# Kernel tuning notes

Hardware: AMD Instinct MI355X
Metric: run time of the kernel (lower is better)

## Reference

```python
import jax, jax.numpy as jnp
import numpy as np

B, N, D, K = 16, 512, 256, 12  # batch, nodes, node_dim, num edge types (4 arg + 4 arg' + punct +/- + no_edges +/-)
ITERATION_STEPS = 1


def setup_inputs() -> dict:
    key = jax.random.key(0)
    ks = jax.random.split(key, 8)
    node = jax.random.normal(ks[0], (B, N, D), dtype=jnp.float32)
    node_mask = jax.random.randint(ks[1], (B, N), 0, 2, dtype=jnp.int32)
    graphs = jax.random.randint(ks[2], (K, B, N, N), 0, 2, dtype=jnp.int32)
    s = 1.0 / np.sqrt(D)
    Ww = jax.random.normal(ks[3], (1, D), dtype=jnp.float32) * s   # _node_weight_fc
    bw = jnp.zeros((1,), dtype=jnp.float32)
    Ws = jax.random.normal(ks[4], (D, D), dtype=jnp.float32) * s   # _self_node_fc
    bs = jnp.zeros((D,), dtype=jnp.float32)
    Wk = jax.random.normal(ks[5], (K, D, D), dtype=jnp.float32) * s  # 12 bias-free per-edge-type linears
    return {"node": node, "Ww": Ww, "bw": bw, "Ws": Ws, "bs": bs, "Wk": Wk,
            "node_mask": node_mask, "graphs": graphs}


def reference(node, Ww, bw, Ws, bs, Wk, node_mask, graphs):
    dt = node.dtype
    mask = node_mask.astype(dt)
    eye = jnp.eye(N, dtype=dt)
    # dd_graph = mask_row * mask_col * (1 - diag)
    dd = mask[:, None, :] * mask[:, :, None] * (1.0 - eye)          # [B,N,N]
    g = dd[None] * graphs.astype(dt)                                # [K,B,N,N] masked adjacencies
    neigh = g.sum(axis=(0, 3))                                      # [B,N] total neighbor count
    neigh = jnp.where(neigh >= 1, neigh, jnp.ones((), dt))

    all_w = []
    for _ in range(ITERATION_STEPS):
        # (1) node relatedness
        w = jax.nn.sigmoid(node @ Ww.T + bw)[..., 0]                # [B,N]
        all_w.append(w)
        self_info = node @ Ws.T + bs                                # [B,N,D]
        # (2) message propagation for all 12 edge types, batched
        trans = jnp.einsum('bnd,ked->kbne', node, Wk)               # [K,B,N,D] per-type linear (x @ W.T)
        wg = w[None, :, None, :] * g                                # [K,B,N,N] masked node weights
        agg = jnp.einsum('kbmn,kbnd->bmd', wg, trans) / neigh[..., None]
        # (3) update
        node = jax.nn.relu(self_info + agg)

    all_weight = jnp.stack(all_w, axis=1)                           # [B,steps,N]
    return node, all_weight
```

## Files before the change

### kernel.cpp

```cpp
#include <hip/hip_runtime.h>
#include <hip/hip_bf16.h>
#include <math.h>

#define BB 16
#define NN 512
#define DD 256
#define KK 12

typedef __bf16 bf16x8 __attribute__((ext_vector_type(8)));
typedef __bf16 bf16x4 __attribute__((ext_vector_type(4)));
typedef float  f32x4  __attribute__((ext_vector_type(4)));

#define WS_WM     0
#define WS_NCNT   32768
#define WS_NODEBF 65536
#define WS_NODET  4259840
#define WS_WKBF   8454144
#define WS_WSBF   10027008
#define WS_T      10158080

__global__ __launch_bounds__(256) void k1_prep(const float* __restrict__ node,
        const float* __restrict__ Ww, const float* __restrict__ bw,
        const int* __restrict__ node_mask,
        float* __restrict__ wm, __bf16* __restrict__ node_bf,
        float* __restrict__ all_w) {
    int t = threadIdx.x;
    int lane = t & 63;
    int row = blockIdx.x * 4 + (t >> 6);
    const float4 nv = *(const float4*)(node + (size_t)row * DD + lane * 4);
    const float4 wv = *(const float4*)(Ww + lane * 4);
    float dot = nv.x*wv.x + nv.y*wv.y + nv.z*wv.z + nv.w*wv.w;
    #pragma unroll
    for (int off = 32; off > 0; off >>= 1) dot += __shfl_xor(dot, off);
    float w = 1.0f / (1.0f + expf(-(dot + bw[0])));
    int mk = node_mask[row];
    if (lane == 0) {
        wm[row]    = w * (float)mk;
        all_w[row] = w;
    }
    bf16x4 nb = {(__bf16)nv.x, (__bf16)nv.y, (__bf16)nv.z, (__bf16)nv.w};
    *(bf16x4*)(node_bf + (size_t)row * DD + lane * 4) = nb;
}

__global__ __launch_bounds__(256) void k1b_convert(const float* __restrict__ Wk,
        const float* __restrict__ Ws, __bf16* __restrict__ Wk_bf, __bf16* __restrict__ Ws_bf) {
    const int KDD = KK * DD * DD;
    int idx = (blockIdx.x * 256 + threadIdx.x) * 4;
    if (idx < KDD) {
        float4 v = *(const float4*)(Wk + idx);
        bf16x4 o = {(__bf16)v.x, (__bf16)v.y, (__bf16)v.z, (__bf16)v.w};
        *(bf16x4*)(Wk_bf + idx) = o;
    } else {
        int j = idx - KDD;
        if (j < DD * DD) {
            float4 v = *(const float4*)(Ws + j);
            bf16x4 o = {(__bf16)v.x, (__bf16)v.y, (__bf16)v.z, (__bf16)v.w};
            *(bf16x4*)(Ws_bf + j) = o;
        }
    }
}

__global__ __launch_bounds__(256) void k2_transpose(const float* __restrict__ node,
        const float* __restrict__ wm, __bf16* __restrict__ dst) {
    __shared__ float tile[64][65];
    int bx = blockIdx.x;
    int b = bx >> 5; int rest = bx & 31; int nt = rest >> 2; int dt = rest & 3;
    int n0 = nt * 64, d0 = dt * 64;
    int t = threadIdx.x;
    #pragma unroll
    for (int i = 0; i < 16; i++) {
        int idx = i * 256 + t;
        int n = idx >> 6, d = idx & 63;
        tile[n][d] = node[((size_t)(b * NN + n0 + n)) * DD + d0 + d];
    }
    __syncthreads();
    #pragma unroll
    for (int i = 0; i < 16; i++) {
        int idx = i * 256 + t;
        int d = idx >> 6, n = idx & 63;
        float w = wm[b * NN + n0 + n];
        dst[((size_t)(b * DD + d0 + d)) * NN + n0 + n] = (__bf16)(tile[n][d] * w);
    }
}

__global__ __launch_bounds__(256) void k4_stageA(const int* __restrict__ graphs,
        const int* __restrict__ node_mask, const __bf16* __restrict__ node_t,
        __bf16* __restrict__ T, int* __restrict__ ncnt) {
    __shared__ __align__(16) __bf16 Asub[64][72];
    int bx = blockIdx.x;
    int mt = bx & 7;
    int kb = bx >> 3;
    int b = kb & 15;
    int k = kb >> 4;
    int m0 = mt * 64;
    int t = threadIdx.x;
    int lane = t & 63;
    int wave = t >> 6;
    int q = lane >> 4;
    int l16 = lane & 15;
    int e0 = wave * 64;

    f32x4 acc[4][4];
    #pragma unroll
    for (int i = 0; i < 4; i++)
        #pragma unroll
        for (int j = 0; j < 4; j++) acc[i][j] = (f32x4){0.f, 0.f, 0.f, 0.f};

    int am = t >> 2;
    int aq = t & 3;
    const int* grow = graphs + ((size_t)((k * BB + b) * NN + m0 + am)) * NN;
    const int* mrow = node_mask + b * NN;
    int mg = m0 + am;
    unsigned cnt = 0;

    for (int n0 = 0; n0 < NN; n0 += 64) {
        #pragma unroll
        for (int i = 0; i < 4; i++) {
            int nbase = n0 + aq * 16 + i * 4;
            int4 g  = *(const int4*)(grow + nbase);
            int4 mk = *(const int4*)(mrow + nbase);
            unsigned p0 = (unsigned)g.x | ((unsigned)g.y << 16);
            unsigned p1 = (unsigned)g.z | ((unsigned)g.w << 16);
            unsigned drel = (unsigned)(mg - nbase);
            if (drel < 4u) {
                unsigned bit = 1u << (16 * (drel & 1));
                if (drel < 2u) p0 &= ~bit; else p1 &= ~bit;
            }
            unsigned mp0 = (unsigned)mk.x | ((unsigned)mk.y << 16);
            unsigned mp1 = (unsigned)mk.z | ((unsigned)mk.w << 16);
            cnt += (p0 & mp0) + (p1 & mp1);
            uint2 st;
            st.x = p0 * 0x3F80u;
            st.y = p1 * 0x3F80u;
            *(uint2*)&Asub[am][aq * 16 + i * 4] = st;
        }
        __syncthreads();
        #pragma unroll
        for (int kk = 0; kk < 2; kk++) {
            bf16x8 af[4], bfr[4];
            #pragma unroll
            for (int fm = 0; fm < 4; fm++)
                af[fm] = *(const bf16x8*)&Asub[fm * 16 + l16][kk * 32 + q * 8];
            #pragma unroll
            for (int fd = 0; fd < 4; fd++)
                bfr[fd] = *(const bf16x8*)(node_t +
                    ((size_t)(b * DD + e0 + fd * 16 + l16)) * NN + n0 + kk * 32 + q * 8);
            #pragma unroll
            for (int fm = 0; fm < 4; fm++)
                #pragma unroll
                for (int fd = 0; fd < 4; fd++)
                    acc[fm][fd] = __builtin_amdgcn_mfma_f32_16x16x32_bf16(
                        af[fm], bfr[fd], acc[fm][fd], 0, 0, 0);
        }
        __syncthreads();
    }

    cnt = (cnt & 0xFFFFu) + (cnt >> 16);
    int ci = (int)cnt;
    ci += __shfl_xor(ci, 1);
    ci += __shfl_xor(ci, 2);
    if (aq == 0) atomicAdd(&ncnt[b * NN + mg], ci);

    #pragma unroll
    for (int fm = 0; fm < 4; fm++)
        #pragma unroll
        for (int fd = 0; fd < 4; fd++) {
            int col = e0 + fd * 16 + l16;
            #pragma unroll
            for (int r = 0; r < 4; r++) {
                int m = m0 + fm * 16 + q * 4 + r;
                T[((size_t)((b * NN + m) * KK + k)) * DD + col] = (__bf16)acc[fm][fd][r];
            }
        }
}

__global__ __launch_bounds__(256) void k5_stageB(const __bf16* __restrict__ T,
        const __bf16* __restrict__ Wk_bf, const __bf16* __restrict__ node_bf,
        const __bf16* __restrict__ Ws_bf, const float* __restrict__ bs,
        const int* __restrict__ ncnt, const int* __restrict__ node_mask,
        float* __restrict__ out) {
    __shared__ float redbuf[64][65];
    int bx = blockIdx.x;
    int b = bx >> 5; int rest = bx & 31; int mt = rest >> 2; int dt = rest & 3;
    int m0 = mt * 64, d0 = dt * 64;
    int t = threadIdx.x;
    int lane = t & 63;
    int wave = t >> 6;
    int q = lane >> 4;
    int l16 = lane & 15;
    int ew = wave * 64;

    f32x4 acc[4][4];
    #pragma unroll
    for (int i = 0; i < 4; i++)
        #pragma unroll
        for (int j = 0; j < 4; j++) acc[i][j] = (f32x4){0.f, 0.f, 0.f, 0.f};

    for (int k = 0; k < KK; k++) {
        #pragma unroll
        for (int kk = 0; kk < 2; kk++) {
            int eoff = ew + kk * 32 + q * 8;
            bf16x8 af[4], bfr[4];
            #pragma unroll
            for (int fm = 0; fm < 4; fm++)
                af[fm] = *(const bf16x8*)(T +
                    ((size_t)(b * NN + m0 + fm * 16 + l16)) * (KK * DD) + k * DD + eoff);
            #pragma unroll
            for (int fd = 0; fd < 4; fd++)
                bfr[fd] = *(const bf16x8*)(Wk_bf +
                    ((size_t)(k * DD + d0 + fd * 16 + l16)) * DD + eoff);
            #pragma unroll
            for (int fm = 0; fm < 4; fm++)
                #pragma unroll
                for (int fd = 0; fd < 4; fd++)
                    acc[fm][fd] = __builtin_amdgcn_mfma_f32_16x16x32_bf16(
                        af[fm], bfr[fd], acc[fm][fd], 0, 0, 0);
        }
    }

    #pragma unroll
    for (int fm = 0; fm < 4; fm++) {
        #pragma unroll
        for (int r = 0; r < 4; r++) {
            int m = m0 + fm * 16 + q * 4 + r;
            int c = ncnt[b * NN + m];
            float s = (float)node_mask[b * NN + m] / (float)(c >= 1 ? c : 1);
            #pragma unroll
            for (int fd = 0; fd < 4; fd++) acc[fm][fd][r] *= s;
        }
    }

    #pragma unroll
    for (int kk = 0; kk < 2; kk++) {
        int eoff = ew + kk * 32 + q * 8;
        bf16x8 af[4], bfr[4];
        #pragma unroll
        for (int fm = 0; fm < 4; fm++)
            af[fm] = *(const bf16x8*)(node_bf +
                ((size_t)(b * NN + m0 + fm * 16 + l16)) * DD + eoff);
        #pragma unroll
        for (int fd = 0; fd < 4; fd++)
            bfr[fd] = *(const bf16x8*)(Ws_bf +
                ((size_t)(d0 + fd * 16 + l16)) * DD + eoff);
        #pragma unroll
        for (int fm = 0; fm < 4; fm++)
            #pragma unroll
            for (int fd = 0; fd < 4; fd++)
                acc[fm][fd] = __builtin_amdgcn_mfma_f32_16x16x32_bf16(
                    af[fm], bfr[fd], acc[fm][fd], 0, 0, 0);
    }

    for (int w = 0; w < 4; w++) {
        if (wave == w) {
            #pragma unroll
            for (int fm = 0; fm < 4; fm++)
                #pragma unroll
                for (int fd = 0; fd < 4; fd++) {
                    int dd2 = fd * 16 + l16;
                    #pragma unroll
                    for (int r = 0; r < 4; r++) {
                        int mm = fm * 16 + q * 4 + r;
                        if (w == 0) redbuf[mm][dd2] = acc[fm][fd][r];
                        else        redbuf[mm][dd2] += acc[fm][fd][r];
                    }
                }
        }
        __syncthreads();
    }

    int row = t >> 2;
    int c0 = (t & 3) * 16;
    #pragma unroll
    for (int j = 0; j < 4; j++) {
        int d = d0 + c0 + j * 4;
        float4 bv = *(const float4*)(bs + d);
        float4 v;
        v.x = fmaxf(redbuf[row][c0 + j * 4 + 0] + bv.x, 0.0f);
        v.y = fmaxf(redbuf[row][c0 + j * 4 + 1] + bv.y, 0.0f);
        v.z = fmaxf(redbuf[row][c0 + j * 4 + 2] + bv.z, 0.0f);
        v.w = fmaxf(redbuf[row][c0 + j * 4 + 3] + bv.w, 0.0f);
        *(float4*)(out + ((size_t)(b * NN + m0 + row)) * DD + d) = v;
    }
}

extern "C" void kernel_launch(void* const* d_in, const int* in_sizes, int n_in,
                              void* d_out, int out_size, void* d_ws, size_t ws_size,
                              hipStream_t stream) {
    const float* node      = (const float*)d_in[0];
    const float* Ww        = (const float*)d_in[1];
    const float* bw        = (const float*)d_in[2];
    const float* Ws        = (const float*)d_in[3];
    const float* bs        = (const float*)d_in[4];
    const float* Wk        = (const float*)d_in[5];
    const int*   node_mask = (const int*)d_in[6];
    const int*   graphs    = (const int*)d_in[7];
    float* out   = (float*)d_out;
    float* all_w = out + (size_t)BB * NN * DD;

    char* ws = (char*)d_ws;
    float*  wm      = (float*)(ws + WS_WM);
    int*    ncnt    = (int*)(ws + WS_NCNT);
    __bf16* node_bf = (__bf16*)(ws + WS_NODEBF);
    __bf16* node_t  = (__bf16*)(ws + WS_NODET);
    __bf16* Wk_bf   = (__bf16*)(ws + WS_WKBF);
    __bf16* Ws_bf   = (__bf16*)(ws + WS_WSBF);
    __bf16* Tbuf    = (__bf16*)(ws + WS_T);

    hipMemsetAsync(ncnt, 0, BB * NN * sizeof(int), stream);
    k1_prep    <<<2048, 256, 0, stream>>>(node, Ww, bw, node_mask, wm, node_bf, all_w);
    k1b_convert<<< 832, 256, 0, stream>>>(Wk, Ws, Wk_bf, Ws_bf);
    k2_transpose<<<512, 256, 0, stream>>>(node, wm, node_t);
    k4_stageA  <<<1536, 256, 0, stream>>>(graphs, node_mask, node_t, Tbuf, ncnt);
    k5_stageB  <<< 512, 256, 0, stream>>>(Tbuf, Wk_bf, node_bf, Ws_bf, bs, ncnt, node_mask, out);
}
```

Baseline: 393.2 us.

## Stage full adjacency row block in LDS upfront and count neighbors via MFMA

Stage A now loads the whole 64x512 masked adjacency tile for a block into shared memory in one pass, using wide coalesced int4 loads with eight loads in flight. After a single barrier it runs all 16 MFMA k-steps without per-chunk syncs. The per-row neighbor count, previously a scalar popcount-style sum against node_mask, is now an extra MFMA against a bf16 mask vector spread across waves and reduced through LDS. Block index order is also changed so the batch index varies fastest. In exchange the kernel uses about 66KB of LDS, which lowers occupancy, and the global loads no longer overlap with compute.

```diff
diff --git a/kernel.cpp b/kernel.cpp
--- a/kernel.cpp
+++ b/kernel.cpp
@@ -13,17 +13,18 @@
 
 #define WS_WM     0
 #define WS_NCNT   32768
-#define WS_NODEBF 65536
-#define WS_NODET  4259840
-#define WS_WKBF   8454144
-#define WS_WSBF   10027008
-#define WS_T      10158080
+#define WS_MASKBF 65536
+#define WS_NODEBF 81920
+#define WS_NODET  4276224
+#define WS_WKBF   8470528
+#define WS_WSBF   10043392
+#define WS_T      10174464
 
 __global__ __launch_bounds__(256) void k1_prep(const float* __restrict__ node,
         const float* __restrict__ Ww, const float* __restrict__ bw,
         const int* __restrict__ node_mask,
-        float* __restrict__ wm, __bf16* __restrict__ node_bf,
-        float* __restrict__ all_w) {
+        float* __restrict__ wm, __bf16* __restrict__ maskbf,
+        __bf16* __restrict__ node_bf, float* __restrict__ all_w) {
     int t = threadIdx.x;
     int lane = t & 63;
     int row = blockIdx.x * 4 + (t >> 6);
@@ -35,8 +36,9 @@
     float w = 1.0f / (1.0f + expf(-(dot + bw[0])));
     int mk = node_mask[row];
     if (lane == 0) {
-        wm[row]    = w * (float)mk;
-        all_w[row] = w;
+        wm[row]     = w * (float)mk;
+        all_w[row]  = w;
+        maskbf[row] = (__bf16)(float)mk;
     }
     bf16x4 nb = {(__bf16)nv.x, (__bf16)nv.y, (__bf16)nv.z, (__bf16)nv.w};
     *(bf16x4*)(node_bf + (size_t)row * DD + lane * 4) = nb;
@@ -84,14 +86,14 @@
 }
 
 __global__ __launch_bounds__(256) void k4_stageA(const int* __restrict__ graphs,
-        const int* __restrict__ node_mask, const __bf16* __restrict__ node_t,
+        const __bf16* __restrict__ maskbf, const __bf16* __restrict__ node_t,
         __bf16* __restrict__ T, int* __restrict__ ncnt) {
-    __shared__ __align__(16) __bf16 Asub[64][72];
+    __shared__ __align__(16) __bf16 Abf[64][520];
+    __shared__ float cntp[4][64];
     int bx = blockIdx.x;
-    int mt = bx & 7;
-    int kb = bx >> 3;
-    int b = kb & 15;
-    int k = kb >> 4;
+    int b  = bx & 15;
+    int mt = (bx >> 4) & 7;
+    int k  = bx >> 7;
     int m0 = mt * 64;
     int t = threadIdx.x;
     int lane = t & 63;
@@ -100,66 +102,79 @@
     int l16 = lane & 15;
     int e0 = wave * 64;
 
+    const int4* gbase = (const int4*)(graphs + ((size_t)((k * BB + b) * NN + m0)) * NN);
+    int colbase = (t * 4) & 511;
+    int rowpar  = t >> 7;
+    #pragma unroll
+    for (int jj = 0; jj < 4; jj++) {
+        int4 g[8];
+        #pragma unroll
+        for (int u = 0; u < 8; u++)
+            g[u] = gbase[(jj * 8 + u) * 256 + t];
+        #pragma unroll
+        for (int u = 0; u < 8; u++) {
+            int row = 2 * (jj * 8 + u) + rowpar;
+            unsigned p0 = (unsigned)g[u].x | ((unsigned)g[u].y << 16);
+            unsigned p1 = (unsigned)g[u].z | ((unsigned)g[u].w << 16);
+            unsigned drel = (unsigned)(m0 + row - colbase);
+            if (drel < 2u)      p0 &= ~(0xFFFFu << (16 * drel));
+            else if (drel < 4u) p1 &= ~(0xFFFFu << (16 * (drel - 2)));
+            uint2 st; st.x = p0 * 0x3F80u; st.y = p1 * 0x3F80u;
+            *(uint2*)&Abf[row][colbase] = st;
+        }
+    }
+    __syncthreads();
+
     f32x4 acc[4][4];
     #pragma unroll
     for (int i = 0; i < 4; i++)
         #pragma unroll
         for (int j = 0; j < 4; j++) acc[i][j] = (f32x4){0.f, 0.f, 0.f, 0.f};
-
-    int am = t >> 2;
-    int aq = t & 3;
-    const int* grow = graphs + ((size_t)((k * BB + b) * NN + m0 + am)) * NN;
-    const int* mrow = node_mask + b * NN;
-    int mg = m0 + am;
-    unsigned cnt = 0;
-
-    for (int n0 = 0; n0 < NN; n0 += 64) {
-        #pragma unroll
-        for (int i = 0; i < 4; i++) {
-            int nbase = n0 + aq * 16 + i * 4;
-            int4 g  = *(const int4*)(grow + nbase);
-            int4 mk = *(const int4*)(mrow + nbase);
-            unsigned p0 = (unsigned)g.x | ((unsigned)g.y << 16);
-            unsigned p1 = (unsigned)g.z | ((unsigned)g.w << 16);
-            unsigned drel = (unsigned)(mg - nbase);
-            if (drel < 4u) {
-                unsigned bit = 1u << (16 * (drel & 1));
-                if (drel < 2u) p0 &= ~bit; else p1 &= ~bit;
-            }
-            unsigned mp0 = (unsigned)mk.x | ((unsigned)mk.y << 16);
-            unsigned mp1 = (unsigned)mk.z | ((unsigned)mk.w << 16);
-            cnt += (p0 & mp0) + (p1 & mp1);
-            uint2 st;
-            st.x = p0 * 0x3F80u;
-            st.y = p1 * 0x3F80u;
-            *(uint2*)&Asub[am][aq * 16 + i * 4] = st;
-        }
-        __syncthreads();
-        #pragma unroll
-        for (int kk = 0; kk < 2; kk++) {
-            bf16x8 af[4], bfr[4];
+    f32x4 accC[4];
+    #pragma unroll
+    for (int i = 0; i < 4; i++) accC[i] = (f32x4){0.f, 0.f, 0.f, 0.f};
+    int cw0 = wave * 4;
+
+    #pragma unroll
+    for (int kk = 0; kk < 16; kk++) {
+        int n0c = kk * 32;
+        bf16x8 af[4], bfr[4];
+        #pragma unroll
+        for (int fm = 0; fm < 4; fm++)
+            af[fm] = *(const bf16x8*)&Abf[fm * 16 + l16][n0c + q * 8];
+        #pragma unroll
+        for (int fd = 0; fd < 4; fd++)
+            bfr[fd] = *(const bf16x8*)(node_t +
+                ((size_t)(b * DD + e0 + fd * 16 + l16)) * NN + n0c + q * 8);
+        #pragma unroll
+        for (int fm = 0; fm < 4; fm++)
+            #pragma unroll
+            for (int fd = 0; fd < 4; fd++)
+                acc[fm][fd] = __builtin_amdgcn_mfma_f32_16x16x32_bf16(
+                    af[fm], bfr[fd], acc[fm][fd], 0, 0, 0);
+        if (kk >= cw0 && kk < cw0 + 4) {
+            bf16x8 bfm = (bf16x8){0,0,0,0,0,0,0,0};
+            if (l16 == 0)
+                bfm = *(const bf16x8*)(maskbf + b * NN + n0c + q * 8);
             #pragma unroll
             for (int fm = 0; fm < 4; fm++)
-                af[fm] = *(const bf16x8*)&Asub[fm * 16 + l16][kk * 32 + q * 8];
-            #pragma unroll
-            for (int fd = 0; fd < 4; fd++)
-                bfr[fd] = *(const bf16x8*)(node_t +
-                    ((size_t)(b * DD + e0 + fd * 16 + l16)) * NN + n0 + kk * 32 + q * 8);
-            #pragma unroll
-            for (int fm = 0; fm < 4; fm++)
-                #pragma unroll
-                for (int fd = 0; fd < 4; fd++)
-                    acc[fm][fd] = __builtin_amdgcn_mfma_f32_16x16x32_bf16(
-                        af[fm], bfr[fd], acc[fm][fd], 0, 0, 0);
-        }
-        __syncthreads();
-    }
-
-    cnt = (cnt & 0xFFFFu) + (cnt >> 16);
-    int ci = (int)cnt;
-    ci += __shfl_xor(ci, 1);
-    ci += __shfl_xor(ci, 2);
-    if (aq == 0) atomicAdd(&ncnt[b * NN + mg], ci);
+                accC[fm] = __builtin_amdgcn_mfma_f32_16x16x32_bf16(
+                    af[fm], bfm, accC[fm], 0, 0, 0);
+        }
+    }
+
+    if (l16 == 0) {
+        #pragma unroll
+        for (int fm = 0; fm < 4; fm++)
+            #pragma unroll
+            for (int r = 0; r < 4; r++)
+                cntp[wave][fm * 16 + q * 4 + r] = accC[fm][r];
+    }
+    __syncthreads();
+    if (t < 64) {
+        float c = cntp[0][t] + cntp[1][t] + cntp[2][t] + cntp[3][t];
+        atomicAdd(&ncnt[b * NN + m0 + t], (int)(c + 0.5f));
+    }
 
     #pragma unroll
     for (int fm = 0; fm < 4; fm++)
@@ -181,7 +196,9 @@
         float* __restrict__ out) {
     __shared__ float redbuf[64][65];
     int bx = blockIdx.x;
-    int b = bx >> 5; int rest = bx & 31; int mt = rest >> 2; int dt = rest & 3;
+    int b = bx & 15;
+    int mt = (bx >> 4) & 7;
+    int dt = bx >> 7;
     int m0 = mt * 64, d0 = dt * 64;
     int t = threadIdx.x;
     int lane = t & 63;
@@ -300,6 +317,7 @@
     char* ws = (char*)d_ws;
     float*  wm      = (float*)(ws + WS_WM);
     int*    ncnt    = (int*)(ws + WS_NCNT);
+    __bf16* maskbf  = (__bf16*)(ws + WS_MASKBF);
     __bf16* node_bf = (__bf16*)(ws + WS_NODEBF);
     __bf16* node_t  = (__bf16*)(ws + WS_NODET);
     __bf16* Wk_bf   = (__bf16*)(ws + WS_WKBF);
@@ -307,9 +325,9 @@
     __bf16* Tbuf    = (__bf16*)(ws + WS_T);
 
     hipMemsetAsync(ncnt, 0, BB * NN * sizeof(int), stream);
-    k1_prep    <<<2048, 256, 0, stream>>>(node, Ww, bw, node_mask, wm, node_bf, all_w);
+    k1_prep    <<<2048, 256, 0, stream>>>(node, Ww, bw, node_mask, wm, maskbf, node_bf, all_w);
     k1b_convert<<< 832, 256, 0, stream>>>(Wk, Ws, Wk_bf, Ws_bf);
     k2_transpose<<<512, 256, 0, stream>>>(node, wm, node_t);
-    k4_stageA  <<<1536, 256, 0, stream>>>(graphs, node_mask, node_t, Tbuf, ncnt);
+    k4_stageA  <<<1536, 256, 0, stream>>>(graphs, maskbf, node_t, Tbuf, ncnt);
     k5_stageB  <<< 512, 256, 0, stream>>>(Tbuf, Wk_bf, node_bf, Ws_bf, bs, ncnt, node_mask, out);
 }
```

After: 405.2 us. 1.03x slower.
